# Performance work log

Hardware: AMD Instinct MI355X
Metric: run time of the kernel (lower is better)

Reference implementation:

```python
import jax, jax.numpy as jnp
import numpy as np

N = 1_000_000
DIM = 64
HID = 64  # max(8, int(dim*hidden_ratio)) with hidden_ratio=1.0
P = 4096  # number of patches
EPS = 1e-5


def setup_inputs() -> dict:
    key = jax.random.key(0)
    ks = jax.random.split(key, 12)
    x = jax.random.normal(ks[0], (N, DIM), dtype=jnp.float32)
    coord = jax.random.uniform(ks[1], (N, 3), dtype=jnp.float32)
    patch_ids = jax.random.randint(ks[2], (N,), 0, P)
    s1 = 1.0 / np.sqrt(3.0)
    s2 = 1.0 / np.sqrt(HID)
    s3 = 1.0 / np.sqrt(DIM)
    W1 = jax.random.uniform(ks[3], (3, HID), jnp.float32, -s1, s1)
    b1 = jax.random.uniform(ks[4], (HID,), jnp.float32, -s1, s1)
    W2 = jax.random.uniform(ks[5], (HID, DIM), jnp.float32, -s2, s2)
    b2 = jax.random.uniform(ks[6], (DIM,), jnp.float32, -s2, s2)
    dw_w = jax.random.uniform(ks[7], (DIM,), jnp.float32, -1.0, 1.0)  # conv1d k=1 groups=dim -> per-channel scale
    dw_b = jax.random.uniform(ks[8], (DIM,), jnp.float32, -1.0, 1.0)
    pw_W = jax.random.uniform(ks[9], (DIM, DIM), jnp.float32, -s3, s3)
    pw_b = jax.random.uniform(ks[10], (DIM,), jnp.float32, -s3, s3)
    ln_g = jnp.ones((DIM,), jnp.float32)
    ln_b = jnp.zeros((DIM,), jnp.float32)
    return dict(x=x, coord=coord, patch_ids=patch_ids, W1=W1, b1=b1, W2=W2,
                b2=b2, dw_w=dw_w, dw_b=dw_b, pw_W=pw_W, pw_b=pw_b,
                ln_g=ln_g, ln_b=ln_b)


def reference(x, coord, patch_ids, W1, b1, W2, b2, dw_w, dw_b, pw_W, pw_b, ln_g, ln_b):
    # segment mean of coords over patches: (P, 3)
    sums = jax.ops.segment_sum(coord, patch_ids, num_segments=P)
    cnt = jax.ops.segment_sum(jnp.ones((coord.shape[0], 1), coord.dtype), patch_ids, num_segments=P)
    centers = sums / jnp.maximum(cnt, 1.0)
    delta = coord - centers[patch_ids]  # (N, 3) gather-broadcast
    # small MLP 3 -> hid -> dim (exact erf GELU, matching torch default)
    pos = jax.nn.gelu(delta @ W1 + b1, approximate=False) @ W2 + b2
    out = x + pos
    # depthwise conv1d k=1 == per-channel affine, then pointwise linear
    y = out * dw_w + dw_b
    out = y @ pw_W + pw_b
    # LayerNorm
    mu = jnp.mean(out, axis=-1, keepdims=True)
    var = jnp.mean(jnp.square(out - mu), axis=-1, keepdims=True)
    return (out - mu) * jax.lax.rsqrt(var + EPS) * ln_g + ln_b
```

## Files before the change

### kernel.cpp

```cpp
#include <hip/hip_runtime.h>
#include <hip/hip_bf16.h>
#include <math.h>

#define NPTS 1000000
#define DIM 64
#define HID 64
#define NPATCH 4096
#define BM 128
#define LDH 72

typedef float f32x4 __attribute__((ext_vector_type(4)));
typedef __bf16 bf16x8 __attribute__((ext_vector_type(8)));
typedef __bf16 bf16x4 __attribute__((ext_vector_type(4)));

#define PB_BLOCKS 64
#define PB_PTS (NPTS / PB_BLOCKS)

__global__ __launch_bounds__(256) void patch_partial(const float* __restrict__ coord,
                                                     const int* __restrict__ ids,
                                                     float* __restrict__ acc4) {
    __shared__ float lacc[NPATCH * 4];
    for (int j = threadIdx.x; j < NPATCH * 4; j += 256) lacc[j] = 0.0f;
    __syncthreads();
    const int start = blockIdx.x * PB_PTS;
    const int end = start + PB_PTS;
    for (int i = start + threadIdx.x; i < end; i += 256) {
        int p = ids[i];
        float cx = coord[3 * i + 0];
        float cy = coord[3 * i + 1];
        float cz = coord[3 * i + 2];
        atomicAdd(&lacc[4 * p + 0], cx);
        atomicAdd(&lacc[4 * p + 1], cy);
        atomicAdd(&lacc[4 * p + 2], cz);
        atomicAdd(&lacc[4 * p + 3], 1.0f);
    }
    __syncthreads();
    for (int j = threadIdx.x; j < NPATCH * 4; j += 256)
        atomicAdd(&acc4[j], lacc[j]);
}

__global__ __launch_bounds__(256, 4) void cpe_main(
    const float* __restrict__ x, const float* __restrict__ coord,
    const int* __restrict__ ids,
    const float* __restrict__ W1, const float* __restrict__ b1,
    const float* __restrict__ W2, const float* __restrict__ b2,
    const float* __restrict__ dww, const float* __restrict__ dwb,
    const float* __restrict__ pwW, const float* __restrict__ pwb,
    const float* __restrict__ lng, const float* __restrict__ lnb,
    const float* __restrict__ acc4, float* __restrict__ out) {

    __shared__ __align__(16) __bf16 sW2t[64 * LDH];
    __shared__ __align__(16) __bf16 sPWt[64 * LDH];
    __shared__ __align__(16) __bf16 sHY[BM * LDH];
    __shared__ float sW1[3 * 64];
    __shared__ __align__(16) float sb1[64], sb2[64], sdww[64], sdwb[64],
                                   spwb[64], slng[64], slnb[64];

    const int tid = threadIdx.x;
    const int lane = tid & 63;
    const int wave = tid >> 6;
    const int block0 = blockIdx.x * BM;
    const int q = lane >> 4;
    const int ln = lane & 15;

    const int prow0 = wave * 32 + ln;
    f32x4 xv[2][4];
    #pragma unroll
    for (int m = 0; m < 2; ++m) {
        int gp = block0 + prow0 + m * 16;
        const float* xr = x + (size_t)gp * 64 + q * 4;
        #pragma unroll
        for (int t = 0; t < 4; ++t)
            xv[m][t] = (gp < NPTS) ? *(const f32x4*)(xr + t * 16)
                                   : (f32x4){0.f, 0.f, 0.f, 0.f};
    }

    if (tid < 192) sW1[tid] = W1[tid];
    if (tid < 64) {
        sb1[tid] = b1[tid];  sb2[tid] = b2[tid];
        sdww[tid] = dww[tid]; sdwb[tid] = dwb[tid];
        spwb[tid] = pwb[tid]; slng[tid] = lng[tid]; slnb[tid] = lnb[tid];
    }
    for (int e = tid; e < 64 * 64; e += 256) {
        int k = e >> 6, n = e & 63;
        sW2t[n * LDH + k] = (__bf16)W2[e];
        sPWt[n * LDH + k] = (__bf16)pwW[e];
    }
    __syncthreads();

    {
        int p = tid & (BM - 1);
        int half = tid >> 7;
        int gp = block0 + p;
        float d0 = 0.f, d1 = 0.f, d2 = 0.f;
        if (gp < NPTS) {
            int pid = ids[gp];
            float4 a = ((const float4*)acc4)[pid];
            float invc = 1.0f / fmaxf(a.w, 1.0f);
            d0 = coord[3 * gp + 0] - a.x * invc;
            d1 = coord[3 * gp + 1] - a.y * invc;
            d2 = coord[3 * gp + 2] - a.z * invc;
        }
        #pragma unroll
        for (int j0 = 0; j0 < 32; j0 += 8) {
            bf16x8 pack;
            #pragma unroll
            for (int u = 0; u < 8; ++u) {
                int j = half * 32 + j0 + u;
                float v = sb1[j] + d0 * sW1[j] + d1 * sW1[64 + j] + d2 * sW1[128 + j];
                v = 0.5f * v * (1.0f + erff(v * 0.70710678118654752f));
                pack[u] = (__bf16)v;
            }
            *(bf16x8*)&sHY[p * LDH + half * 32 + j0] = pack;
        }
    }
    __syncthreads();

    f32x4 acc[2][4];
    #pragma unroll
    for (int m = 0; m < 2; ++m)
        #pragma unroll
        for (int t = 0; t < 4; ++t)
            acc[m][t] = (f32x4){0.f, 0.f, 0.f, 0.f};

    #pragma unroll
    for (int ks = 0; ks < 2; ++ks) {
        bf16x8 hw[2], wf[4];
        #pragma unroll
        for (int m = 0; m < 2; ++m)
            hw[m] = *(const bf16x8*)&sHY[(prow0 + m * 16) * LDH + ks * 32 + q * 8];
        #pragma unroll
        for (int t = 0; t < 4; ++t)
            wf[t] = *(const bf16x8*)&sW2t[(t * 16 + ln) * LDH + ks * 32 + q * 8];
        #pragma unroll
        for (int m = 0; m < 2; ++m)
            #pragma unroll
            for (int t = 0; t < 4; ++t)
                acc[m][t] = __builtin_amdgcn_mfma_f32_16x16x32_bf16(wf[t], hw[m], acc[m][t], 0, 0, 0);
    }
    __syncthreads();

    #pragma unroll
    for (int m = 0; m < 2; ++m) {
        #pragma unroll
        for (int t = 0; t < 4; ++t) {
            int c0 = t * 16 + q * 4;
            f32x4 o = xv[m][t] + acc[m][t] + *(const f32x4*)&sb2[c0];
            f32x4 y = o * *(const f32x4*)&sdww[c0] + *(const f32x4*)&sdwb[c0];
            bf16x4 yb;
            #pragma unroll
            for (int j = 0; j < 4; ++j) yb[j] = (__bf16)y[j];
            *(bf16x4*)&sHY[(prow0 + m * 16) * LDH + c0] = yb;
        }
    }
    __syncthreads();

    #pragma unroll
    for (int m = 0; m < 2; ++m)
        #pragma unroll
        for (int t = 0; t < 4; ++t)
            acc[m][t] = (f32x4){0.f, 0.f, 0.f, 0.f};

    #pragma unroll
    for (int ks = 0; ks < 2; ++ks) {
        bf16x8 yw[2], wf[4];
        #pragma unroll
        for (int m = 0; m < 2; ++m)
            yw[m] = *(const bf16x8*)&sHY[(prow0 + m * 16) * LDH + ks * 32 + q * 8];
        #pragma unroll
        for (int t = 0; t < 4; ++t)
            wf[t] = *(const bf16x8*)&sPWt[(t * 16 + ln) * LDH + ks * 32 + q * 8];
        #pragma unroll
        for (int m = 0; m < 2; ++m)
            #pragma unroll
            for (int t = 0; t < 4; ++t)
                acc[m][t] = __builtin_amdgcn_mfma_f32_16x16x32_bf16(wf[t], yw[m], acc[m][t], 0, 0, 0);
    }

    #pragma unroll
    for (int m = 0; m < 2; ++m) {
        int gp = block0 + prow0 + m * 16;
        f32x4 v[4];
        float s = 0.f, ss = 0.f;
        #pragma unroll
        for (int t = 0; t < 4; ++t) {
            int c0 = t * 16 + q * 4;
            v[t] = acc[m][t] + *(const f32x4*)&spwb[c0];
            #pragma unroll
            for (int j = 0; j < 4; ++j) { s += v[t][j]; ss += v[t][j] * v[t][j]; }
        }
        s += __shfl_xor(s, 16);  s += __shfl_xor(s, 32);
        ss += __shfl_xor(ss, 16); ss += __shfl_xor(ss, 32);
        float mu = s * (1.0f / 64.0f);
        float rs = rsqrtf(ss * (1.0f / 64.0f) - mu * mu + 1e-5f);
        if (gp < NPTS) {
            float* op = out + (size_t)gp * 64;
            #pragma unroll
            for (int t = 0; t < 4; ++t) {
                int c0 = t * 16 + q * 4;
                f32x4 g = *(const f32x4*)&slng[c0];
                f32x4 b = *(const f32x4*)&slnb[c0];
                f32x4 o = (v[t] - mu) * rs * g + b;
                *(f32x4*)(op + c0) = o;
            }
        }
    }
}

extern "C" void kernel_launch(void* const* d_in, const int* in_sizes, int n_in,
                              void* d_out, int out_size, void* d_ws, size_t ws_size,
                              hipStream_t stream) {
    const float* x     = (const float*)d_in[0];
    const float* coord = (const float*)d_in[1];
    const int*   ids   = (const int*)d_in[2];
    const float* W1    = (const float*)d_in[3];
    const float* b1    = (const float*)d_in[4];
    const float* W2    = (const float*)d_in[5];
    const float* b2    = (const float*)d_in[6];
    const float* dww   = (const float*)d_in[7];
    const float* dwb   = (const float*)d_in[8];
    const float* pwW   = (const float*)d_in[9];
    const float* pwb   = (const float*)d_in[10];
    const float* lng   = (const float*)d_in[11];
    const float* lnb   = (const float*)d_in[12];
    float* outp = (float*)d_out;
    float* acc4 = (float*)d_ws;

    hipMemsetAsync(d_ws, 0, NPATCH * 4 * sizeof(float), stream);
    patch_partial<<<PB_BLOCKS, 256, 0, stream>>>(coord, ids, acc4);
    cpe_main<<<(NPTS + BM - 1) / BM, 256, 0, stream>>>(
        x, coord, ids, W1, b1, W2, b2, dww, dwb, pwW, pwb, lng, lnb, acc4, outp);
}
```

Before: 570.9 us.

## Pre-swizzle weights globally, two-stage patch reduction, plane-major LDS layout

```diff
diff --git a/kernel.cpp b/kernel.cpp
--- a/kernel.cpp
+++ b/kernel.cpp
@@ -3,56 +3,81 @@
 #include <math.h>
 
 #define NPTS 1000000
-#define DIM 64
-#define HID 64
 #define NPATCH 4096
 #define BM 128
-#define LDH 72
 
 typedef float f32x4 __attribute__((ext_vector_type(4)));
 typedef __bf16 bf16x8 __attribute__((ext_vector_type(8)));
 typedef __bf16 bf16x4 __attribute__((ext_vector_type(4)));
 
-#define PB_BLOCKS 64
+#define PB_BLOCKS 250
 #define PB_PTS (NPTS / PB_BLOCKS)
 
+#define SPLANE (BM * 8 + 16)
+
+__device__ __align__(16) float  g_acc4[NPATCH * 4];
+__device__ __align__(16) __bf16 g_w2f[4096];
+__device__ __align__(16) __bf16 g_pwf[4096];
+__device__ __align__(16) float  g_part[PB_BLOCKS * NPATCH * 4];
+
+__global__ __launch_bounds__(256) void transpose_w(const float* __restrict__ W2,
+                                                   const float* __restrict__ pwW) {
+    const float* src = (blockIdx.x == 0) ? W2 : pwW;
+    __bf16* dst = (blockIdx.x == 0) ? g_w2f : g_pwf;
+    for (int e = threadIdx.x; e < 4096; e += 256) {
+        int j = e & 7;
+        int lane = (e >> 3) & 63;
+        int ft = e >> 9;
+        int ks = ft >> 2, t = ft & 3;
+        int q = lane >> 4, ln = lane & 15;
+        dst[e] = (__bf16)src[(ks * 32 + q * 8 + j) * 64 + t * 16 + ln];
+    }
+}
+
 __global__ __launch_bounds__(256) void patch_partial(const float* __restrict__ coord,
-                                                     const int* __restrict__ ids,
-                                                     float* __restrict__ acc4) {
-    __shared__ float lacc[NPATCH * 4];
-    for (int j = threadIdx.x; j < NPATCH * 4; j += 256) lacc[j] = 0.0f;
+                                                     const int* __restrict__ ids) {
+    __shared__ float lacc[4 * NPATCH];
+    for (int j = threadIdx.x; j < 4 * NPATCH; j += 256) lacc[j] = 0.0f;
     __syncthreads();
     const int start = blockIdx.x * PB_PTS;
     const int end = start + PB_PTS;
     for (int i = start + threadIdx.x; i < end; i += 256) {
         int p = ids[i];
-        float cx = coord[3 * i + 0];
-        float cy = coord[3 * i + 1];
-        float cz = coord[3 * i + 2];
-        atomicAdd(&lacc[4 * p + 0], cx);
-        atomicAdd(&lacc[4 * p + 1], cy);
-        atomicAdd(&lacc[4 * p + 2], cz);
-        atomicAdd(&lacc[4 * p + 3], 1.0f);
-    }
-    __syncthreads();
-    for (int j = threadIdx.x; j < NPATCH * 4; j += 256)
-        atomicAdd(&acc4[j], lacc[j]);
-}
-
-__global__ __launch_bounds__(256, 4) void cpe_main(
+        atomicAdd(&lacc[0 * NPATCH + p], coord[3 * i + 0]);
+        atomicAdd(&lacc[1 * NPATCH + p], coord[3 * i + 1]);
+        atomicAdd(&lacc[2 * NPATCH + p], coord[3 * i + 2]);
+        atomicAdd(&lacc[3 * NPATCH + p], 1.0f);
+    }
+    __syncthreads();
+    float* dst = g_part + (size_t)blockIdx.x * 4 * NPATCH;
+    for (int j = threadIdx.x; j < 4 * NPATCH; j += 256) {
+        int p = j >> 2, c = j & 3;
+        dst[j] = lacc[c * NPATCH + p];
+    }
+}
+
+__global__ __launch_bounds__(256) void patch_reduce() {
+    int j = blockIdx.x * 256 + threadIdx.x;
+    float s = 0.0f;
+    #pragma unroll 10
+    for (int k = 0; k < PB_BLOCKS; ++k)
+        s += g_part[(size_t)k * 4 * NPATCH + j];
+    g_acc4[j] = s;
+}
+
+__global__ __launch_bounds__(256, 8) void cpe_main(
     const float* __restrict__ x, const float* __restrict__ coord,
     const int* __restrict__ ids,
     const float* __restrict__ W1, const float* __restrict__ b1,
-    const float* __restrict__ W2, const float* __restrict__ b2,
+    const float* __restrict__ b2,
     const float* __restrict__ dww, const float* __restrict__ dwb,
-    const float* __restrict__ pwW, const float* __restrict__ pwb,
+    const float* __restrict__ pwb,
     const float* __restrict__ lng, const float* __restrict__ lnb,
-    const float* __restrict__ acc4, float* __restrict__ out) {
-
-    __shared__ __align__(16) __bf16 sW2t[64 * LDH];
-    __shared__ __align__(16) __bf16 sPWt[64 * LDH];
-    __shared__ __align__(16) __bf16 sHY[BM * LDH];
-    __shared__ float sW1[3 * 64];
+    float* __restrict__ out) {
+
+    __shared__ __align__(16) __bf16 sH[8 * SPLANE];
+    __shared__ __align__(16) float scoord[BM * 3];
+    __shared__ float sW1[192];
     __shared__ __align__(16) float sb1[64], sb2[64], sdww[64], sdwb[64],
                                    spwb[64], slng[64], slnb[64];
 
@@ -62,18 +87,7 @@
     const int block0 = blockIdx.x * BM;
     const int q = lane >> 4;
     const int ln = lane & 15;
-
     const int prow0 = wave * 32 + ln;
-    f32x4 xv[2][4];
-    #pragma unroll
-    for (int m = 0; m < 2; ++m) {
-        int gp = block0 + prow0 + m * 16;
-        const float* xr = x + (size_t)gp * 64 + q * 4;
-        #pragma unroll
-        for (int t = 0; t < 4; ++t)
-            xv[m][t] = (gp < NPTS) ? *(const f32x4*)(xr + t * 16)
-                                   : (f32x4){0.f, 0.f, 0.f, 0.f};
-    }
 
     if (tid < 192) sW1[tid] = W1[tid];
     if (tid < 64) {
@@ -81,10 +95,11 @@
         sdww[tid] = dww[tid]; sdwb[tid] = dwb[tid];
         spwb[tid] = pwb[tid]; slng[tid] = lng[tid]; slnb[tid] = lnb[tid];
     }
-    for (int e = tid; e < 64 * 64; e += 256) {
-        int k = e >> 6, n = e & 63;
-        sW2t[n * LDH + k] = (__bf16)W2[e];
-        sPWt[n * LDH + k] = (__bf16)pwW[e];
+    if (tid < 96) {
+        int g4 = (block0 * 3) / 4 + tid;
+        f32x4 c = (g4 < (NPTS * 3) / 4) ? ((const f32x4*)coord)[g4]
+                                        : (f32x4){0.f, 0.f, 0.f, 0.f};
+        *(f32x4*)&scoord[tid * 4] = c;
     }
     __syncthreads();
 
@@ -95,11 +110,11 @@
         float d0 = 0.f, d1 = 0.f, d2 = 0.f;
         if (gp < NPTS) {
             int pid = ids[gp];
-            float4 a = ((const float4*)acc4)[pid];
+            float4 a = ((const float4*)g_acc4)[pid];
             float invc = 1.0f / fmaxf(a.w, 1.0f);
-            d0 = coord[3 * gp + 0] - a.x * invc;
-            d1 = coord[3 * gp + 1] - a.y * invc;
-            d2 = coord[3 * gp + 2] - a.z * invc;
+            d0 = scoord[3 * p + 0] - a.x * invc;
+            d1 = scoord[3 * p + 1] - a.y * invc;
+            d2 = scoord[3 * p + 2] - a.z * invc;
         }
         #pragma unroll
         for (int j0 = 0; j0 < 32; j0 += 8) {
@@ -111,7 +126,8 @@
                 v = 0.5f * v * (1.0f + erff(v * 0.70710678118654752f));
                 pack[u] = (__bf16)v;
             }
-            *(bf16x8*)&sHY[p * LDH + half * 32 + j0] = pack;
+            int g = half * 4 + (j0 >> 3);
+            *(bf16x8*)&sH[g * SPLANE + p * 8] = pack;
         }
     }
     __syncthreads();
@@ -128,15 +144,26 @@
         bf16x8 hw[2], wf[4];
         #pragma unroll
         for (int m = 0; m < 2; ++m)
-            hw[m] = *(const bf16x8*)&sHY[(prow0 + m * 16) * LDH + ks * 32 + q * 8];
-        #pragma unroll
-        for (int t = 0; t < 4; ++t)
-            wf[t] = *(const bf16x8*)&sW2t[(t * 16 + ln) * LDH + ks * 32 + q * 8];
+            hw[m] = *(const bf16x8*)&sH[(ks * 4 + q) * SPLANE + (prow0 + m * 16) * 8];
+        #pragma unroll
+        for (int t = 0; t < 4; ++t)
+            wf[t] = *(const bf16x8*)&g_w2f[((ks * 4 + t) * 64 + lane) * 8];
         #pragma unroll
         for (int m = 0; m < 2; ++m)
             #pragma unroll
             for (int t = 0; t < 4; ++t)
                 acc[m][t] = __builtin_amdgcn_mfma_f32_16x16x32_bf16(wf[t], hw[m], acc[m][t], 0, 0, 0);
+    }
+
+    f32x4 xv[2][4];
+    #pragma unroll
+    for (int m = 0; m < 2; ++m) {
+        int gp = block0 + prow0 + m * 16;
+        const float* xr = x + (size_t)gp * 64 + q * 4;
+        #pragma unroll
+        for (int t = 0; t < 4; ++t)
+            xv[m][t] = (gp < NPTS) ? *(const f32x4*)(xr + t * 16)
+                                   : (f32x4){0.f, 0.f, 0.f, 0.f};
     }
     __syncthreads();
 
@@ -150,7 +177,8 @@
             bf16x4 yb;
             #pragma unroll
             for (int j = 0; j < 4; ++j) yb[j] = (__bf16)y[j];
-            *(bf16x4*)&sHY[(prow0 + m * 16) * LDH + c0] = yb;
+            int g = 2 * t + (q >> 1);
+            *(bf16x4*)&sH[g * SPLANE + (prow0 + m * 16) * 8 + (q & 1) * 4] = yb;
         }
     }
     __syncthreads();
@@ -166,10 +194,10 @@
         bf16x8 yw[2], wf[4];
         #pragma unroll
         for (int m = 0; m < 2; ++m)
-            yw[m] = *(const bf16x8*)&sHY[(prow0 + m * 16) * LDH + ks * 32 + q * 8];
-        #pragma unroll
-        for (int t = 0; t < 4; ++t)
-            wf[t] = *(const bf16x8*)&sPWt[(t * 16 + ln) * LDH + ks * 32 + q * 8];
+            yw[m] = *(const bf16x8*)&sH[(ks * 4 + q) * SPLANE + (prow0 + m * 16) * 8];
+        #pragma unroll
+        for (int t = 0; t < 4; ++t)
+            wf[t] = *(const bf16x8*)&g_pwf[((ks * 4 + t) * 64 + lane) * 8];
         #pragma unroll
         for (int m = 0; m < 2; ++m)
             #pragma unroll
@@ -201,7 +229,7 @@
                 f32x4 g = *(const f32x4*)&slng[c0];
                 f32x4 b = *(const f32x4*)&slnb[c0];
                 f32x4 o = (v[t] - mu) * rs * g + b;
-                *(f32x4*)(op + c0) = o;
+                __builtin_nontemporal_store(o, (f32x4*)(op + c0));
             }
         }
     }
@@ -224,10 +252,11 @@
     const float* lng   = (const float*)d_in[11];
     const float* lnb   = (const float*)d_in[12];
     float* outp = (float*)d_out;
-    float* acc4 = (float*)d_ws;
-
-    hipMemsetAsync(d_ws, 0, NPATCH * 4 * sizeof(float), stream);
-    patch_partial<<<PB_BLOCKS, 256, 0, stream>>>(coord, ids, acc4);
+    (void)d_ws; (void)ws_size;
+
+    transpose_w<<<2, 256, 0, stream>>>(W2, pwW);
+    patch_partial<<<PB_BLOCKS, 256, 0, stream>>>(coord, ids);
+    patch_reduce<<<NPATCH * 4 / 256, 256, 0, stream>>>();
     cpe_main<<<(NPTS + BM - 1) / BM, 256, 0, stream>>>(
-        x, coord, ids, W1, b1, W2, b2, dww, dwb, pwW, pwb, lng, lnb, acc4, outp);
-}
+        x, coord, ids, W1, b1, b2, dww, dwb, pwb, lng, lnb, outp);
+}
```

Result: faster. 527.8 us (-7.5%).
